# Performance work log

Hardware: AMD Instinct MI355X
Metric: run time of the kernel (lower is better)

The kernel has to match this reference:

```python
import jax, jax.numpy as jnp
import numpy as np

N_CLUSTERS = 1024


def setup_inputs() -> dict:
    key = jax.random.key(0)
    k1, k2 = jax.random.split(key)
    batch = jax.random.normal(k1, (262144, 64), dtype=jnp.float32)
    centroids = jax.random.normal(k2, (N_CLUSTERS, 64), dtype=jnp.float32)
    return {"batch": batch, "centroids": centroids}


def reference(batch, centroids):
    x_sq = jnp.sum(batch * batch, axis=1, keepdims=True)          # [N, 1]
    c_sq = jnp.sum(centroids * centroids, axis=1)                 # [K]
    cross = batch @ centroids.T                                   # [N, K]
    distances = x_sq - 2.0 * cross + c_sq[None, :]
    assignments = jnp.argmin(distances, axis=1)                   # [N] int
    # Counts and sums via scatter-add (avoids materializing one-hot [N, K])
    batch_cluster_counts = jnp.zeros((N_CLUSTERS,), dtype=jnp.int32).at[assignments].add(1)
    batch_cluster_sums = jax.ops.segment_sum(batch, assignments, num_segments=N_CLUSTERS)  # [K, D]
    return (assignments, batch_cluster_counts, batch_cluster_sums)
```

## Files before the change

### kernel.cpp

```cpp
#include <hip/hip_runtime.h>
#include <float.h>

#define N_PTS 262144
#define K_CL  1024
#define D     64
#define PTS_PER_WAVE   64
#define WAVES_PER_BLK  16
#define PTS_PER_BLK    (PTS_PER_WAVE * WAVES_PER_BLK)
#define NTILE 8
#define MARGIN_S 0.5f
#define CAND_CAP 6

typedef _Float16 f16;
typedef _Float16 half8 __attribute__((ext_vector_type(8)));
typedef float    f32x4 __attribute__((ext_vector_type(4)));

__global__ __launch_bounds__(256) void prep_kernel(const float* __restrict__ cent,
                                                   float* __restrict__ csq,
                                                   float* __restrict__ csqhn,
                                                   f16* __restrict__ cent16) {
    int k = blockIdx.x * 256 + threadIdx.x;
    if (k >= K_CL) return;
    const float* row = &cent[(size_t)k * D];
    float s = 0.f;
    #pragma unroll
    for (int d = 0; d < D; ++d) s = fmaf(row[d], row[d], s);
    csq[k]   = s;
    csqhn[k] = -0.5f * s;
    int sw = k & 7;
    #pragma unroll
    for (int ch = 0; ch < 8; ++ch) {
        half8 h;
        #pragma unroll
        for (int e = 0; e < 8; ++e) h[e] = (f16)row[ch * 8 + e];
        *reinterpret_cast<half8*>(&cent16[(size_t)k * D + (size_t)((ch ^ sw) * 8)]) = h;
    }
}

__device__ __forceinline__ float exact_dist(const float* __restrict__ xr,
                                            const float* __restrict__ cr,
                                            float xsq, float cs) {
    float dot = 0.f;
    #pragma unroll
    for (int d = 0; d < D; ++d) dot = fmaf(xr[d], cr[d], dot);
    return (xsq - 2.0f * dot) + cs;
}

__device__ __forceinline__ half8 point_frag(const float* __restrict__ batch,
                                            int prow, int chunk) {
    const float* src = &batch[(size_t)prow * D + chunk * 8];
    float4 u0 = *reinterpret_cast<const float4*>(src);
    float4 u1 = *reinterpret_cast<const float4*>(src + 4);
    half8 h;
    h[0] = (f16)u0.x; h[1] = (f16)u0.y; h[2] = (f16)u0.z; h[3] = (f16)u0.w;
    h[4] = (f16)u1.x; h[5] = (f16)u1.y; h[6] = (f16)u1.z; h[7] = (f16)u1.w;
    return h;
}

__device__ __forceinline__ float vmax4(const f32x4& a) {
    return fmaxf(fmaxf(a.x, a.y), fmaxf(a.z, a.w));
}

__device__ __forceinline__ void collect(const f32x4& a, float thr, int cbase, int& cnt,
                                        int& s0, int& s1, int& s2, int& s3, int& s4, int& s5) {
    if (vmax4(a) >= thr) {
        #pragma unroll
        for (int r = 0; r < 4; ++r) {
            if (a[r] >= thr) {
                int c = cbase + r;
                if      (cnt == 0) s0 = c;
                else if (cnt == 1) s1 = c;
                else if (cnt == 2) s2 = c;
                else if (cnt == 3) s3 = c;
                else if (cnt == 4) s4 = c;
                else if (cnt == 5) s5 = c;
                cnt++;
            }
        }
    }
}

__device__ __forceinline__ void resolve(const float* __restrict__ batch,
                                        const float* __restrict__ cent,
                                        const float* __restrict__ csq,
                                        int prow, int hi, int cnt,
                                        int s0, int s1, int s2, int s3, int s4, int s5,
                                        float& bd, int& bi) {
    bd = FLT_MAX; bi = 0x7fffffff;
    if (cnt == 0) return;
    const float* xr = &batch[(size_t)prow * D];
    float xsq = 0.f;
    #pragma unroll
    for (int d = 0; d < D; ++d) xsq = fmaf(xr[d], xr[d], xsq);
    if (cnt <= CAND_CAP) {
        #pragma unroll
        for (int r = 0; r < CAND_CAP; ++r) {
            int c = (r == 0) ? s0 : (r == 1) ? s1 : (r == 2) ? s2
                  : (r == 3) ? s3 : (r == 4) ? s4 : s5;
            if (r < cnt) {
                float dd = exact_dist(xr, &cent[(size_t)c * D], xsq, csq[c]);
                if (dd < bd || (dd == bd && c < bi)) { bd = dd; bi = c; }
            }
        }
    } else {
        for (int t16 = 0; t16 < 64; ++t16) {
            #pragma unroll
            for (int r = 0; r < 4; ++r) {
                int c = t16 * 16 + hi * 4 + r;
                float dd = exact_dist(xr, &cent[(size_t)c * D], xsq, csq[c]);
                if (dd < bd || (dd == bd && c < bi)) { bd = dd; bi = c; }
            }
        }
    }
}

__global__ __launch_bounds__(1024, 4) void assign_kernel(
    const float* __restrict__ batch,
    const f16*   __restrict__ cent16,
    const float* __restrict__ csq,
    const float* __restrict__ csqhn,
    const float* __restrict__ cent,
    float* __restrict__ out_assign,
    float* __restrict__ ps_base,
    float* __restrict__ cs_base,
    int split_mask)
{
    __shared__ f16   C16[K_CL * D];
    __shared__ __align__(16) float CH[K_CL];

    const int tid   = threadIdx.x;
    const int wave  = tid >> 6;
    const int lane  = tid & 63;
    const int lo    = lane & 15;
    const int hi    = lane >> 4;
    const int wbase = (blockIdx.x * WAVES_PER_BLK + wave) * PTS_PER_WAVE;

    #pragma unroll
    for (int it = 0; it < 8; ++it) {
        int u = tid + 1024 * it;
        *reinterpret_cast<half8*>(&C16[u * 8]) =
            *reinterpret_cast<const half8*>(&cent16[(size_t)u * 8]);
    }
    CH[tid] = csqhn[tid];
    __syncthreads();

    const int pr0 = wbase + 0 * 16 + lo;
    const int pr1 = wbase + 1 * 16 + lo;
    const int pr2 = wbase + 2 * 16 + lo;
    const int pr3 = wbase + 3 * 16 + lo;

    const half8 p0a = point_frag(batch, pr0, hi), p0b = point_frag(batch, pr0, 4 + hi);
    const half8 p1a = point_frag(batch, pr1, hi), p1b = point_frag(batch, pr1, 4 + hi);
    const half8 p2a = point_frag(batch, pr2, hi), p2b = point_frag(batch, pr2, 4 + hi);
    const half8 p3a = point_frag(batch, pr3, hi), p3b = point_frag(batch, pr3, 4 + hi);

    float m0 = -FLT_MAX, m1 = -FLT_MAX, m2 = -FLT_MAX, m3 = -FLT_MAX;
    for (int t = 0; t < NTILE; ++t) {
        const int base = t * 128;
        #pragma unroll
        for (int m = 0; m < 8; ++m) {
            const int row = base + m * 16 + lo;
            const int sw  = row & 7;
            const half8 cf0 = *reinterpret_cast<const half8*>(&C16[row * D + ((hi     ^ sw) * 8)]);
            const half8 cf1 = *reinterpret_cast<const half8*>(&C16[row * D + (((4+hi) ^ sw) * 8)]);
            const f32x4 ch  = *reinterpret_cast<const f32x4*>(&CH[base + m * 16 + hi * 4]);
            f32x4 a0 = ch, a1 = ch, a2 = ch, a3 = ch;
            a0 = __builtin_amdgcn_mfma_f32_16x16x32_f16(cf0, p0a, a0, 0, 0, 0);
            a0 = __builtin_amdgcn_mfma_f32_16x16x32_f16(cf1, p0b, a0, 0, 0, 0);
            a1 = __builtin_amdgcn_mfma_f32_16x16x32_f16(cf0, p1a, a1, 0, 0, 0);
            a1 = __builtin_amdgcn_mfma_f32_16x16x32_f16(cf1, p1b, a1, 0, 0, 0);
            a2 = __builtin_amdgcn_mfma_f32_16x16x32_f16(cf0, p2a, a2, 0, 0, 0);
            a2 = __builtin_amdgcn_mfma_f32_16x16x32_f16(cf1, p2b, a2, 0, 0, 0);
            a3 = __builtin_amdgcn_mfma_f32_16x16x32_f16(cf0, p3a, a3, 0, 0, 0);
            a3 = __builtin_amdgcn_mfma_f32_16x16x32_f16(cf1, p3b, a3, 0, 0, 0);
            m0 = fmaxf(m0, vmax4(a0));
            m1 = fmaxf(m1, vmax4(a1));
            m2 = fmaxf(m2, vmax4(a2));
            m3 = fmaxf(m3, vmax4(a3));
        }
    }
    m0 = fmaxf(m0, __shfl_xor(m0, 16)); m0 = fmaxf(m0, __shfl_xor(m0, 32));
    m1 = fmaxf(m1, __shfl_xor(m1, 16)); m1 = fmaxf(m1, __shfl_xor(m1, 32));
    m2 = fmaxf(m2, __shfl_xor(m2, 16)); m2 = fmaxf(m2, __shfl_xor(m2, 32));
    m3 = fmaxf(m3, __shfl_xor(m3, 16)); m3 = fmaxf(m3, __shfl_xor(m3, 32));
    const float t0 = m0 - MARGIN_S, t1 = m1 - MARGIN_S,
                t2 = m2 - MARGIN_S, t3 = m3 - MARGIN_S;

    int n0 = 0, n1 = 0, n2 = 0, n3 = 0;
    int a0c0=0,a0c1=0,a0c2=0,a0c3=0,a0c4=0,a0c5=0;
    int a1c0=0,a1c1=0,a1c2=0,a1c3=0,a1c4=0,a1c5=0;
    int a2c0=0,a2c1=0,a2c2=0,a2c3=0,a2c4=0,a2c5=0;
    int a3c0=0,a3c1=0,a3c2=0,a3c3=0,a3c4=0,a3c5=0;

    for (int t = 0; t < NTILE; ++t) {
        const int base = t * 128;
        #pragma unroll
        for (int m = 0; m < 8; ++m) {
            const int row = base + m * 16 + lo;
            const int sw  = row & 7;
            const half8 cf0 = *reinterpret_cast<const half8*>(&C16[row * D + ((hi     ^ sw) * 8)]);
            const half8 cf1 = *reinterpret_cast<const half8*>(&C16[row * D + (((4+hi) ^ sw) * 8)]);
            const f32x4 ch  = *reinterpret_cast<const f32x4*>(&CH[base + m * 16 + hi * 4]);
            f32x4 a0 = ch, a1 = ch, a2 = ch, a3 = ch;
            a0 = __builtin_amdgcn_mfma_f32_16x16x32_f16(cf0, p0a, a0, 0, 0, 0);
            a0 = __builtin_amdgcn_mfma_f32_16x16x32_f16(cf1, p0b, a0, 0, 0, 0);
            a1 = __builtin_amdgcn_mfma_f32_16x16x32_f16(cf0, p1a, a1, 0, 0, 0);
            a1 = __builtin_amdgcn_mfma_f32_16x16x32_f16(cf1, p1b, a1, 0, 0, 0);
            a2 = __builtin_amdgcn_mfma_f32_16x16x32_f16(cf0, p2a, a2, 0, 0, 0);
            a2 = __builtin_amdgcn_mfma_f32_16x16x32_f16(cf1, p2b, a2, 0, 0, 0);
            a3 = __builtin_amdgcn_mfma_f32_16x16x32_f16(cf0, p3a, a3, 0, 0, 0);
            a3 = __builtin_amdgcn_mfma_f32_16x16x32_f16(cf1, p3b, a3, 0, 0, 0);
            const int cbase = base + m * 16 + hi * 4;
            collect(a0, t0, cbase, n0, a0c0, a0c1, a0c2, a0c3, a0c4, a0c5);
            collect(a1, t1, cbase, n1, a1c0, a1c1, a1c2, a1c3, a1c4, a1c5);
            collect(a2, t2, cbase, n2, a2c0, a2c1, a2c2, a2c3, a2c4, a2c5);
            collect(a3, t3, cbase, n3, a3c0, a3c1, a3c2, a3c3, a3c4, a3c5);
        }
    }

    float bd0, bd1, bd2, bd3;
    int   bi0, bi1, bi2, bi3;
    resolve(batch, cent, csq, pr0, hi, n0, a0c0, a0c1, a0c2, a0c3, a0c4, a0c5, bd0, bi0);
    resolve(batch, cent, csq, pr1, hi, n1, a1c0, a1c1, a1c2, a1c3, a1c4, a1c5, bd1, bi1);
    resolve(batch, cent, csq, pr2, hi, n2, a2c0, a2c1, a2c2, a2c3, a2c4, a2c5, bd2, bi2);
    resolve(batch, cent, csq, pr3, hi, n3, a3c0, a3c1, a3c2, a3c3, a3c4, a3c5, bd3, bi3);

    #pragma unroll
    for (int off = 16; off <= 32; off <<= 1) {
        float od; int oi;
        od = __shfl_xor(bd0, off); oi = __shfl_xor(bi0, off);
        if (od < bd0 || (od == bd0 && oi < bi0)) { bd0 = od; bi0 = oi; }
        od = __shfl_xor(bd1, off); oi = __shfl_xor(bi1, off);
        if (od < bd1 || (od == bd1 && oi < bi1)) { bd1 = od; bi1 = oi; }
        od = __shfl_xor(bd2, off); oi = __shfl_xor(bi2, off);
        if (od < bd2 || (od == bd2 && oi < bi2)) { bd2 = od; bi2 = oi; }
        od = __shfl_xor(bd3, off); oi = __shfl_xor(bi3, off);
        if (od < bd3 || (od == bd3 && oi < bi3)) { bd3 = od; bi3 = oi; }
    }

    if (hi == 0) {
        out_assign[pr0] = (float)bi0;
        out_assign[pr1] = (float)bi1;
        out_assign[pr2] = (float)bi2;
        out_assign[pr3] = (float)bi3;
    }

    const int split = (blockIdx.x * WAVES_PER_BLK + wave) & split_mask;
    float* ps = ps_base + (size_t)split * K_CL * D;
    float* cs = cs_base + (size_t)split * K_CL;
    #pragma unroll 4
    for (int s = 0; s < 4; ++s) {
        int bis = (s == 0) ? bi0 : (s == 1) ? bi1 : (s == 2) ? bi2 : bi3;
        for (int p = 0; p < 16; ++p) {
            int a = __shfl(bis, p);
            int pt = wbase + s * 16 + p;
            float v = batch[(size_t)pt * D + lane];
            atomicAdd(&ps[(size_t)a * D + lane], v);
            if (lane == 0) atomicAdd(&cs[a], 1.0f);
        }
    }
}

__global__ __launch_bounds__(256) void reduce_kernel(
    const float* __restrict__ partial,
    const float* __restrict__ cnt_partial,
    float* __restrict__ out_counts,
    float* __restrict__ out_sums,
    int nsplit)
{
    int idx = blockIdx.x * 256 + threadIdx.x;
    if (idx < K_CL * D) {
        float s = 0.f;
        for (int e = 0; e < nsplit; ++e) s += partial[(size_t)e * K_CL * D + idx];
        out_sums[idx] = s;
    } else if (idx < K_CL * D + K_CL) {
        int c = idx - K_CL * D;
        float s = 0.f;
        for (int e = 0; e < nsplit; ++e) s += cnt_partial[e * K_CL + c];
        out_counts[c] = s;
    }
}

extern "C" void kernel_launch(void* const* d_in, const int* in_sizes, int n_in,
                              void* d_out, int out_size, void* d_ws, size_t ws_size,
                              hipStream_t stream) {
    const float* batch = (const float*)d_in[0];
    const float* cent  = (const float*)d_in[1];
    float* out        = (float*)d_out;
    float* out_assign = out;
    float* out_counts = out + N_PTS;
    float* out_sums   = out + N_PTS + K_CL;

    char* ws = (char*)d_ws;
    float* csq    = (float*)ws;
    float* csqhn  = (float*)(ws + 4096);
    f16*   cent16 = (f16*)(ws + 8192);
    float* partial = (float*)(ws + 8192 + 131072);

    int nsplit = 0;
    for (int ns = 32; ns >= 2; ns >>= 1) {
        size_t need = 8192 + 131072 +
                      (size_t)ns * K_CL * D * 4 + (size_t)ns * K_CL * 4;
        if (ws_size >= need) { nsplit = ns; break; }
    }

    prep_kernel<<<K_CL / 256, 256, 0, stream>>>(cent, csq, csqhn, cent16);

    if (nsplit > 0) {
        float* cnt_partial = partial + (size_t)nsplit * K_CL * D;
        hipMemsetAsync(partial, 0,
                       (size_t)(nsplit * K_CL * D + nsplit * K_CL) * sizeof(float), stream);
        assign_kernel<<<N_PTS / PTS_PER_BLK, 1024, 0, stream>>>(
            batch, cent16, csq, csqhn, cent, out_assign,
            partial, cnt_partial, nsplit - 1);
        reduce_kernel<<<(K_CL * D + K_CL + 255) / 256, 256, 0, stream>>>(
            partial, cnt_partial, out_counts, out_sums, nsplit);
    } else {
        hipMemsetAsync(out_counts, 0, (size_t)(K_CL + K_CL * D) * sizeof(float), stream);
        assign_kernel<<<N_PTS / PTS_PER_BLK, 1024, 0, stream>>>(
            batch, cent16, csq, csqhn, cent, out_assign,
            out_sums, out_counts, 0);
    }
}
```

Before: 191.0 us.

## Split centroid set across two blocks per point group, merge in separate scatter kernel

The assign kernel now handles half of the centroids per block: it holds 64 KB of fp16 centroids in LDS instead of 128 KB and raises launch bounds to 8 waves/SIMD. Per-half best distances and indices are written to workspace, and a new merge_scatter kernel picks the winner and does the atomic scatter-add of sums and counts. The aim is more resident blocks per CU and more latency hiding. The cost is twice the point-fragment loads, an extra kernel launch, and a round trip through global memory for the partial results. The fallback path is replaced by a simple brute-force kernel.

```diff
diff --git a/kernel.cpp b/kernel.cpp
--- a/kernel.cpp
+++ b/kernel.cpp
@@ -7,7 +7,9 @@
 #define PTS_PER_WAVE   64
 #define WAVES_PER_BLK  16
 #define PTS_PER_BLK    (PTS_PER_WAVE * WAVES_PER_BLK)
-#define NTILE 8
+#define NGRP (N_PTS / PTS_PER_BLK)
+#define HKC  (K_CL / 2)
+#define NTILE_H 4
 #define MARGIN_S 0.5f
 #define CAND_CAP 6
 
@@ -83,7 +85,7 @@
 __device__ __forceinline__ void resolve(const float* __restrict__ batch,
                                         const float* __restrict__ cent,
                                         const float* __restrict__ csq,
-                                        int prow, int hi, int cnt,
+                                        int prow, int hi, int cofs, int cnt,
                                         int s0, int s1, int s2, int s3, int s4, int s5,
                                         float& bd, int& bi) {
     bd = FLT_MAX; bi = 0x7fffffff;
@@ -103,10 +105,10 @@
             }
         }
     } else {
-        for (int t16 = 0; t16 < 64; ++t16) {
+        for (int t16 = 0; t16 < HKC / 16; ++t16) {
             #pragma unroll
             for (int r = 0; r < 4; ++r) {
-                int c = t16 * 16 + hi * 4 + r;
+                int c = cofs + t16 * 16 + hi * 4 + r;
                 float dd = exact_dist(xr, &cent[(size_t)c * D], xsq, csq[c]);
                 if (dd < bd || (dd == bd && c < bi)) { bd = dd; bi = c; }
             }
@@ -114,34 +116,35 @@
     }
 }
 
-__global__ __launch_bounds__(1024, 4) void assign_kernel(
+__global__ __launch_bounds__(1024, 8) void assign_half_kernel(
     const float* __restrict__ batch,
     const f16*   __restrict__ cent16,
     const float* __restrict__ csq,
     const float* __restrict__ csqhn,
     const float* __restrict__ cent,
-    float* __restrict__ out_assign,
-    float* __restrict__ ps_base,
-    float* __restrict__ cs_base,
-    int split_mask)
-{
-    __shared__ f16   C16[K_CL * D];
-    __shared__ __align__(16) float CH[K_CL];
+    float* __restrict__ bdv,
+    int*   __restrict__ biv)
+{
+    __shared__ __align__(16) f16   C16[HKC * D];
+    __shared__ __align__(16) float CH[HKC];
 
     const int tid   = threadIdx.x;
     const int wave  = tid >> 6;
     const int lane  = tid & 63;
     const int lo    = lane & 15;
     const int hi    = lane >> 4;
-    const int wbase = (blockIdx.x * WAVES_PER_BLK + wave) * PTS_PER_WAVE;
-
-    #pragma unroll
-    for (int it = 0; it < 8; ++it) {
+    const int half  = blockIdx.x & 1;
+    const int pgrp  = blockIdx.x >> 1;
+    const int cofs  = half * HKC;
+    const int wbase = (pgrp * WAVES_PER_BLK + wave) * PTS_PER_WAVE;
+
+    #pragma unroll
+    for (int it = 0; it < 4; ++it) {
         int u = tid + 1024 * it;
         *reinterpret_cast<half8*>(&C16[u * 8]) =
-            *reinterpret_cast<const half8*>(&cent16[(size_t)u * 8]);
-    }
-    CH[tid] = csqhn[tid];
+            *reinterpret_cast<const half8*>(&cent16[((size_t)cofs * D / 8 + u) * 8]);
+    }
+    if (tid < HKC) CH[tid] = csqhn[cofs + tid];
     __syncthreads();
 
     const int pr0 = wbase + 0 * 16 + lo;
@@ -155,7 +158,7 @@
     const half8 p3a = point_frag(batch, pr3, hi), p3b = point_frag(batch, pr3, 4 + hi);
 
     float m0 = -FLT_MAX, m1 = -FLT_MAX, m2 = -FLT_MAX, m3 = -FLT_MAX;
-    for (int t = 0; t < NTILE; ++t) {
+    for (int t = 0; t < NTILE_H; ++t) {
         const int base = t * 128;
         #pragma unroll
         for (int m = 0; m < 8; ++m) {
@@ -192,7 +195,7 @@
     int a2c0=0,a2c1=0,a2c2=0,a2c3=0,a2c4=0,a2c5=0;
     int a3c0=0,a3c1=0,a3c2=0,a3c3=0,a3c4=0,a3c5=0;
 
-    for (int t = 0; t < NTILE; ++t) {
+    for (int t = 0; t < NTILE_H; ++t) {
         const int base = t * 128;
         #pragma unroll
         for (int m = 0; m < 8; ++m) {
@@ -210,7 +213,7 @@
             a2 = __builtin_amdgcn_mfma_f32_16x16x32_f16(cf1, p2b, a2, 0, 0, 0);
             a3 = __builtin_amdgcn_mfma_f32_16x16x32_f16(cf0, p3a, a3, 0, 0, 0);
             a3 = __builtin_amdgcn_mfma_f32_16x16x32_f16(cf1, p3b, a3, 0, 0, 0);
-            const int cbase = base + m * 16 + hi * 4;
+            const int cbase = cofs + base + m * 16 + hi * 4;
             collect(a0, t0, cbase, n0, a0c0, a0c1, a0c2, a0c3, a0c4, a0c5);
             collect(a1, t1, cbase, n1, a1c0, a1c1, a1c2, a1c3, a1c4, a1c5);
             collect(a2, t2, cbase, n2, a2c0, a2c1, a2c2, a2c3, a2c4, a2c5);
@@ -220,10 +223,10 @@
 
     float bd0, bd1, bd2, bd3;
     int   bi0, bi1, bi2, bi3;
-    resolve(batch, cent, csq, pr0, hi, n0, a0c0, a0c1, a0c2, a0c3, a0c4, a0c5, bd0, bi0);
-    resolve(batch, cent, csq, pr1, hi, n1, a1c0, a1c1, a1c2, a1c3, a1c4, a1c5, bd1, bi1);
-    resolve(batch, cent, csq, pr2, hi, n2, a2c0, a2c1, a2c2, a2c3, a2c4, a2c5, bd2, bi2);
-    resolve(batch, cent, csq, pr3, hi, n3, a3c0, a3c1, a3c2, a3c3, a3c4, a3c5, bd3, bi3);
+    resolve(batch, cent, csq, pr0, hi, cofs, n0, a0c0, a0c1, a0c2, a0c3, a0c4, a0c5, bd0, bi0);
+    resolve(batch, cent, csq, pr1, hi, cofs, n1, a1c0, a1c1, a1c2, a1c3, a1c4, a1c5, bd1, bi1);
+    resolve(batch, cent, csq, pr2, hi, cofs, n2, a2c0, a2c1, a2c2, a2c3, a2c4, a2c5, bd2, bi2);
+    resolve(batch, cent, csq, pr3, hi, cofs, n3, a3c0, a3c1, a3c2, a3c3, a3c4, a3c5, bd3, bi3);
 
     #pragma unroll
     for (int off = 16; off <= 32; off <<= 1) {
@@ -239,25 +242,44 @@
     }
 
     if (hi == 0) {
-        out_assign[pr0] = (float)bi0;
-        out_assign[pr1] = (float)bi1;
-        out_assign[pr2] = (float)bi2;
-        out_assign[pr3] = (float)bi3;
-    }
-
-    const int split = (blockIdx.x * WAVES_PER_BLK + wave) & split_mask;
-    float* ps = ps_base + (size_t)split * K_CL * D;
-    float* cs = cs_base + (size_t)split * K_CL;
-    #pragma unroll 4
-    for (int s = 0; s < 4; ++s) {
-        int bis = (s == 0) ? bi0 : (s == 1) ? bi1 : (s == 2) ? bi2 : bi3;
-        for (int p = 0; p < 16; ++p) {
-            int a = __shfl(bis, p);
-            int pt = wbase + s * 16 + p;
-            float v = batch[(size_t)pt * D + lane];
-            atomicAdd(&ps[(size_t)a * D + lane], v);
-            if (lane == 0) atomicAdd(&cs[a], 1.0f);
-        }
+        const size_t ho = (size_t)half * N_PTS;
+        bdv[ho + pr0] = bd0;  biv[ho + pr0] = bi0;
+        bdv[ho + pr1] = bd1;  biv[ho + pr1] = bi1;
+        bdv[ho + pr2] = bd2;  biv[ho + pr2] = bi2;
+        bdv[ho + pr3] = bd3;  biv[ho + pr3] = bi3;
+    }
+}
+
+__global__ __launch_bounds__(256) void merge_scatter_kernel(
+    const float* __restrict__ batch,
+    const float* __restrict__ bdv,
+    const int*   __restrict__ biv,
+    float* __restrict__ out_assign,
+    float* __restrict__ ps_base,
+    float* __restrict__ cs_base,
+    int split_mask)
+{
+    const int tid   = threadIdx.x;
+    const int wave  = tid >> 6;
+    const int lane  = tid & 63;
+    const int gw    = blockIdx.x * 4 + wave;
+    const int wbase = gw * 64;
+    const int pt    = wbase + lane;
+
+    const float dA = bdv[pt];
+    const float dB = bdv[N_PTS + pt];
+    const int   iA = biv[pt];
+    const int   iB = biv[N_PTS + pt];
+    const int a = (dB < dA || (dB == dA && iB < iA)) ? iB : iA;
+    out_assign[pt] = (float)a;
+
+    float* ps = ps_base + (size_t)(gw & split_mask) * K_CL * D;
+    float* cs = cs_base + (size_t)(gw & split_mask) * K_CL;
+    for (int p = 0; p < 64; ++p) {
+        int ac = __shfl(a, p);
+        float v = batch[(size_t)(wbase + p) * D + lane];
+        atomicAdd(&ps[(size_t)ac * D + lane], v);
+        if (lane == 0) atomicAdd(&cs[ac], 1.0f);
     }
 }
 
@@ -281,6 +303,46 @@
     }
 }
 
+__global__ __launch_bounds__(256) void assign_bruteforce_kernel(
+    const float* __restrict__ batch,
+    const float* __restrict__ cent,
+    float* __restrict__ out_assign)
+{
+    const int p = blockIdx.x * 256 + threadIdx.x;
+    if (p >= N_PTS) return;
+    const float* xr = &batch[(size_t)p * D];
+    float xsq = 0.f;
+    #pragma unroll
+    for (int d = 0; d < D; ++d) xsq = fmaf(xr[d], xr[d], xsq);
+    float bd = FLT_MAX; int bi = 0;
+    for (int c = 0; c < K_CL; ++c) {
+        const float* cr = &cent[(size_t)c * D];
+        float dot = 0.f, cs = 0.f;
+        #pragma unroll
+        for (int d = 0; d < D; ++d) { dot = fmaf(xr[d], cr[d], dot); cs = fmaf(cr[d], cr[d], cs); }
+        float dd = (xsq - 2.0f * dot) + cs;
+        if (dd < bd) { bd = dd; bi = c; }
+    }
+    out_assign[p] = (float)bi;
+}
+
+__global__ __launch_bounds__(256) void scatter_atomic_kernel(
+    const float* __restrict__ batch,
+    const float* __restrict__ assignF,
+    float* __restrict__ out_counts,
+    float* __restrict__ out_sums)
+{
+    const int gwave = (blockIdx.x * 256 + threadIdx.x) >> 6;
+    const int lane  = threadIdx.x & 63;
+    #pragma unroll 4
+    for (int it = 0; it < 16; ++it) {
+        int p = gwave * 16 + it;
+        int a = (int)assignF[p];
+        if (lane == 0) atomicAdd(&out_counts[a], 1.0f);
+        atomicAdd(&out_sums[(size_t)a * D + lane], batch[(size_t)p * D + lane]);
+    }
+}
+
 extern "C" void kernel_launch(void* const* d_in, const int* in_sizes, int n_in,
                               void* d_out, int out_size, void* d_ws, size_t ws_size,
                               hipStream_t stream) {
@@ -295,30 +357,32 @@
     float* csq    = (float*)ws;
     float* csqhn  = (float*)(ws + 4096);
     f16*   cent16 = (f16*)(ws + 8192);
-    float* partial = (float*)(ws + 8192 + 131072);
-
+    float* bdv    = (float*)(ws + 8192 + 131072);
+    int*   biv    = (int*)((char*)bdv + (size_t)2 * N_PTS * 4);
+    float* partial = (float*)((char*)biv + (size_t)2 * N_PTS * 4);
+
+    const size_t base_need = 8192 + 131072 + (size_t)4 * N_PTS * 4;
     int nsplit = 0;
     for (int ns = 32; ns >= 2; ns >>= 1) {
-        size_t need = 8192 + 131072 +
-                      (size_t)ns * K_CL * D * 4 + (size_t)ns * K_CL * 4;
+        size_t need = base_need + (size_t)ns * K_CL * D * 4 + (size_t)ns * K_CL * 4;
         if (ws_size >= need) { nsplit = ns; break; }
     }
-
-    prep_kernel<<<K_CL / 256, 256, 0, stream>>>(cent, csq, csqhn, cent16);
 
     if (nsplit > 0) {
         float* cnt_partial = partial + (size_t)nsplit * K_CL * D;
-        hipMemsetAsync(partial, 0,
-                       (size_t)(nsplit * K_CL * D + nsplit * K_CL) * sizeof(float), stream);
-        assign_kernel<<<N_PTS / PTS_PER_BLK, 1024, 0, stream>>>(
-            batch, cent16, csq, csqhn, cent, out_assign,
-            partial, cnt_partial, nsplit - 1);
+        prep_kernel<<<K_CL / 256, 256, 0, stream>>>(cent, csq, csqhn, cent16);
+        (void)hipMemsetAsync(partial, 0,
+                (size_t)(nsplit * K_CL * D + nsplit * K_CL) * sizeof(float), stream);
+        assign_half_kernel<<<NGRP * 2, 1024, 0, stream>>>(
+            batch, cent16, csq, csqhn, cent, bdv, biv);
+        merge_scatter_kernel<<<N_PTS / (64 * 4), 256, 0, stream>>>(
+            batch, bdv, biv, out_assign, partial, cnt_partial, nsplit - 1);
         reduce_kernel<<<(K_CL * D + K_CL + 255) / 256, 256, 0, stream>>>(
             partial, cnt_partial, out_counts, out_sums, nsplit);
     } else {
-        hipMemsetAsync(out_counts, 0, (size_t)(K_CL + K_CL * D) * sizeof(float), stream);
-        assign_kernel<<<N_PTS / PTS_PER_BLK, 1024, 0, stream>>>(
-            batch, cent16, csq, csqhn, cent, out_assign,
-            out_sums, out_counts, 0);
-    }
-}
+        (void)hipMemsetAsync(out_counts, 0, (size_t)(K_CL + K_CL * D) * sizeof(float), stream);
+        assign_bruteforce_kernel<<<N_PTS / 256, 256, 0, stream>>>(batch, cent, out_assign);
+        scatter_atomic_kernel<<<N_PTS / (16 * 4), 256, 0, stream>>>(
+            batch, out_assign, out_counts, out_sums);
+    }
+}
```

Result: slower. 487.3 us (+155.1%).
